# Performance work log

Measured on AMD Instinct MI355X. Metric: run time of the kernel, lower is better.

The kernel has to match this reference:

```python
import jax, jax.numpy as jnp
import numpy as np

D_MODEL = 1024
NUM_HEADS = 16
HEAD_DIM = D_MODEL // NUM_HEADS
B, T = 4, 2048


def setup_inputs() -> dict:
    key = jax.random.key(0)
    ks = jax.random.split(key, 11)
    s = 0.02
    return {
        "q": jax.random.normal(ks[0], (B, T, D_MODEL), jnp.float32),
        "k": jax.random.normal(ks[1], (B, T, D_MODEL), jnp.float32),
        "v": jax.random.normal(ks[2], (B, T, D_MODEL), jnp.float32),
        "Wq": jax.random.normal(ks[3], (D_MODEL, D_MODEL), jnp.float32) * s,
        "bq": jnp.zeros((D_MODEL,), jnp.float32),
        "Wk": jax.random.normal(ks[4], (D_MODEL, D_MODEL), jnp.float32) * s,
        "bk": jnp.zeros((D_MODEL,), jnp.float32),
        "Wv": jax.random.normal(ks[5], (D_MODEL, D_MODEL), jnp.float32) * s,
        "bv": jnp.zeros((D_MODEL,), jnp.float32),
        "Wo": jax.random.normal(ks[6], (D_MODEL, D_MODEL), jnp.float32) * s,
        "bo": jnp.zeros((D_MODEL,), jnp.float32),
    }


def reference(q, k, v, Wq, bq, Wk, bk, Wv, bv, Wo, bo):
    Bq, Tq, _ = q.shape
    Tk = k.shape[1]
    # Linear projections then split heads: [B, H, T, Dh]
    qh = (q @ Wq + bq).reshape(Bq, Tq, NUM_HEADS, HEAD_DIM).transpose(0, 2, 1, 3)
    kh = (k @ Wk + bk).reshape(Bq, Tk, NUM_HEADS, HEAD_DIM).transpose(0, 2, 1, 3)
    vh = (v @ Wv + bv).reshape(Bq, Tk, NUM_HEADS, HEAD_DIM).transpose(0, 2, 1, 3)
    scale = 1.0 / jnp.sqrt(jnp.asarray(HEAD_DIM, qh.dtype))
    scores = jnp.einsum("bhqd,bhkd->bhqk", qh, kh) * scale  # [B,H,Tq,Tk]
    attn = jax.nn.softmax(scores, axis=-1)
    # dropout p=0.0 (eval) -> identity
    out = jnp.einsum("bhqk,bhkd->bhqd", attn, vh)  # [B,H,Tq,Dh]
    out = out.transpose(0, 2, 1, 3).reshape(Bq, Tq, D_MODEL)
    return out @ Wo + bo
```

## Files before the change

kernel.cpp:

```cpp
#include <hip/hip_runtime.h>
#include <cstdint>

#define DEV static __device__ __forceinline__

typedef unsigned short u16;
typedef unsigned int u32;
typedef __attribute__((ext_vector_type(8))) _Float16 half8;
typedef __attribute__((ext_vector_type(4))) float f32x4;
typedef __attribute__((ext_vector_type(4))) unsigned short u16x4;

DEV u16 f2h_bits(float f) {
  _Float16 h = (_Float16)f;
  union { _Float16 h; u16 u; } cv; cv.h = h; return cv.u;
}

DEV u32 pack2h(float a, float b) {
  union { __fp16 __attribute__((ext_vector_type(2))) h; u32 u; } cv;
  cv.h = __builtin_amdgcn_cvt_pkrtz(a, b);
  return cv.u;
}

#define EXP2 __builtin_amdgcn_exp2f

DEV void async_cp16(const void* g, void* l) {
  __builtin_amdgcn_global_load_lds(
      (const __attribute__((address_space(1))) void*)g,
      (__attribute__((address_space(3))) void*)l, 16, 0, 0);
}

__global__ void cvt_f16(const float4* __restrict__ in, u16* __restrict__ out) {
  const int i = blockIdx.x * 256 + threadIdx.x;
  float4 f = in[i];
  u16x4 u;
  u.x = f2h_bits(f.x); u.y = f2h_bits(f.y); u.z = f2h_bits(f.z); u.w = f2h_bits(f.w);
  *(u16x4*)(out + i * 4) = u;
}

struct TParams { const float* W[4]; u16* out[4]; };

__global__ void tcvt4(TParams p) {
  __shared__ float tile[32][33];
  const int w = blockIdx.x >> 10;
  const int bidx = blockIdx.x & 1023;
  const float* __restrict__ Wf = p.W[w];
  u16* __restrict__ Wt = p.out[w];
  const int bx = bidx & 31, by = bidx >> 5;
  const int tx = threadIdx.x & 31, ty = threadIdx.x >> 5;
#pragma unroll
  for (int r = 0; r < 32; r += 8)
    tile[ty + r][tx] = Wf[(by * 32 + ty + r) * 1024 + bx * 32 + tx];
  __syncthreads();
#pragma unroll
  for (int r = 0; r < 32; r += 8)
    Wt[(bx * 32 + ty + r) * 1024 + by * 32 + tx] = f2h_bits(tile[tx][ty + r]);
}

template<int EPI, typename OutT>
DEV void gemm_body(const u16* __restrict__ A, const u16* __restrict__ Bt,
                   const float* __restrict__ bias, OutT* __restrict__ out,
                   u16 (*As)[8192], u16 (*Bs)[8192])
{
  const int tid = threadIdx.x;
  const int wave = tid >> 6, lane = tid & 63;
  const int l15 = lane & 15, lg = lane >> 4;
  const int bid = ((blockIdx.x & 7) << 6) | (blockIdx.x >> 3);
  const int bm = bid >> 3, bn = bid & 7;
  const int m0 = bm * 128, n0 = bn * 128;
  const int wr = wave >> 1, wc = wave & 1;

  const f32x4 fz = {0.f, 0.f, 0.f, 0.f};
  f32x4 acc[4][4];
#pragma unroll
  for (int m = 0; m < 4; ++m)
#pragma unroll
    for (int n = 0; n < 4; ++n) acc[m][n] = fz;

  const char* srcA[4]; const char* srcB[4]; int dstAB[4];
#pragma unroll
  for (int j = 0; j < 4; ++j) {
    const int x = (j * 256 + tid) * 16;
    const int row = x >> 7, colb = x & 127;
    const int pc = colb ^ ((row & 7) << 4);
    srcA[j] = (const char*)A  + (size_t)(m0 + row) * 2048 + pc;
    srcB[j] = (const char*)Bt + (size_t)(n0 + row) * 2048 + pc;
    dstAB[j] = x;
  }

#define STAGE_G(buf, T)                                                     \
  do {                                                                      \
    _Pragma("unroll") for (int j = 0; j < 4; ++j)                           \
      async_cp16(srcA[j] + (size_t)(T) * 128, (char*)As[buf] + dstAB[j]);   \
    _Pragma("unroll") for (int j = 0; j < 4; ++j)                           \
      async_cp16(srcB[j] + (size_t)(T) * 128, (char*)Bs[buf] + dstAB[j]);   \
  } while (0)

  STAGE_G(0, 0);
  asm volatile("s_waitcnt vmcnt(0)" ::: "memory");
  __builtin_amdgcn_s_barrier();
  __builtin_amdgcn_sched_barrier(0);

#define GEMM_IT(T, BR, BS)                                                  \
  do {                                                                      \
    if ((T) < 15) STAGE_G(BS, (T) + 1);                                     \
    half8 af[2][4], bf[2][4];                                               \
    _Pragma("unroll") for (int kk = 0; kk < 2; ++kk)                        \
      _Pragma("unroll") for (int m = 0; m < 4; ++m) {                       \
        const int row = wr * 64 + m * 16 + l15;                             \
        af[kk][m] = *(const half8*)((const char*)As[BR] +                   \
            ((row * 128 + kk * 64 + lg * 16) ^ ((row & 7) << 4)));          \
      }                                                                     \
    _Pragma("unroll") for (int kk = 0; kk < 2; ++kk)                        \
      _Pragma("unroll") for (int n = 0; n < 4; ++n) {                       \
        const int row = wc * 64 + n * 16 + l15;                             \
        bf[kk][n] = *(const half8*)((const char*)Bs[BR] +                   \
            ((row * 128 + kk * 64 + lg * 16) ^ ((row & 7) << 4)));          \
      }                                                                     \
    _Pragma("unroll") for (int kk = 0; kk < 2; ++kk)                        \
      _Pragma("unroll") for (int m = 0; m < 4; ++m)                         \
        _Pragma("unroll") for (int n = 0; n < 4; ++n)                       \
          acc[m][n] = __builtin_amdgcn_mfma_f32_16x16x32_f16(af[kk][m], bf[kk][n], acc[m][n], 0, 0, 0); \
    if ((T) < 15) {                                                         \
      asm volatile("s_waitcnt vmcnt(0)" ::: "memory");                      \
      __builtin_amdgcn_s_barrier();                                         \
      __builtin_amdgcn_sched_barrier(0);                                    \
    }                                                                       \
  } while (0)

  for (int tb = 0; tb < 16; tb += 2) {
    GEMM_IT(tb,     0, 1);
    GEMM_IT(tb + 1, 1, 0);
  }
#undef GEMM_IT
#undef STAGE_G

#pragma unroll
  for (int m = 0; m < 4; ++m) {
    const int Rb = m0 + wr * 64 + m * 16 + lg * 4;
#pragma unroll
    for (int n = 0; n < 4; ++n) {
      const int C = n0 + wc * 64 + n * 16 + l15;
      const float bv = bias[C];
#pragma unroll
      for (int i = 0; i < 4; ++i) {
        const int R = Rb + i;
        const float vv = acc[m][n][i] + bv;
        if (EPI == 3) {
          ((float*)out)[(size_t)R * 1024 + C] = vv;
        } else {
          const int b = R >> 11, t = R & 2047, hh = C >> 6, d = C & 63;
          if (EPI == 0)
            ((u16*)out)[((b * 16 + hh) * 2048 + t) * 64 + d] = f2h_bits(vv * 0.18033688f);
          else if (EPI == 1)
            ((u16*)out)[((b * 16 + hh) * 2048 + t) * 64 + d] = f2h_bits(vv);
          else
            ((u16*)out)[((b * 16 + hh) * 64 + d) * 2048 + t] = f2h_bits(vv);
        }
      }
    }
  }
}

template<int EPI>
__launch_bounds__(256, 2)
__global__ void gemm_proj(const u16* __restrict__ A, const u16* __restrict__ Bt,
                          const float* __restrict__ bias, u16* __restrict__ out)
{
  __shared__ u16 As[2][8192];
  __shared__ u16 Bs[2][8192];
  gemm_body<EPI, u16>(A, Bt, bias, out, As, Bs);
}

__launch_bounds__(256, 2)
__global__ void gemm_o(const u16* __restrict__ A, const u16* __restrict__ Bt,
                       const float* __restrict__ bias, float* __restrict__ out)
{
  __shared__ u16 As[2][8192];
  __shared__ u16 Bs[2][8192];
  gemm_body<3, float>(A, Bt, bias, out, As, Bs);
}

__launch_bounds__(512)
__global__ void attn_kernel(const u16* __restrict__ qh, const u16* __restrict__ kh,
                            const u16* __restrict__ vt, u16* __restrict__ O)
{
  __shared__ u16 SM[32768];
  const int tid = threadIdx.x, wave = tid >> 6, lane = tid & 63;
  const int l15 = lane & 15, lg = lane >> 4;
  const int swz = ((blockIdx.x & 7) << 6) | (blockIdx.x >> 3);
  const int bh = swz >> 3;
  const int q0 = (swz & 7) << 8;
  const int b = bh >> 4, h = bh & 15;

  const char* qbase = (const char*)(qh + (size_t)(bh * 2048 + q0) * 64);
  const char* kbase = (const char*)(kh + (size_t)bh * 2048 * 64);
  const char* vbase = (const char*)(vt + (size_t)bh * 64 * 2048);

  char* Kbuf[4] = { (char*)SM,         (char*)SM + 8192,
                    (char*)SM + 16384, (char*)SM + 24576 };
  char* Vbuf[4] = { (char*)SM + 32768, (char*)SM + 40960,
                    (char*)SM + 49152, (char*)SM + 57344 };

  const bool isK = wave < 4;
  const char* ksrc[2]; int kdst[2];
  const char* vsrc[2]; int vdstA[2], vdstB[2];
#pragma unroll
  for (int j = 0; j < 2; ++j) {
    if (isK) {
      const int yb = wave * 2048 + j * 1024 + lane * 16;
      const int row = yb >> 7;
      ksrc[j] = kbase + (yb ^ ((row & 7) << 4));
      kdst[j] = yb;
      vsrc[j] = nullptr; vdstA[j] = vdstB[j] = 0;
    } else {
      const int u = (wave - 4) * 128 + j * 64 + lane;
      const int d = u >> 3, a = u & 7;
      vsrc[j] = vbase + (size_t)d * 4096 + a * 16;
      const int n = a >> 1;
      const int s1 = 32 * (n >> 1) + 16 * (a & 1) + 4 * (n & 1);
      const int sw = (d & 7) << 4;
      vdstA[j] = (d * 128 + 2 * s1) ^ sw;
      vdstB[j] = (d * 128 + 2 * s1 + 16) ^ sw;
      ksrc[j] = nullptr; kdst[j] = 0;
    }
  }

#pragma unroll
  for (int j = 0; j < 4; ++j) {
    const int x = j * 8192 + tid * 16;
    const int row = x >> 7;
    async_cp16(qbase + (x ^ ((row & 7) << 4)), (char*)SM + x);
  }
  __syncthreads();
  half8 aq[2][2];
#pragma unroll
  for (int G = 0; G < 2; ++G) {
    const int qr = wave * 32 + G * 16 + l15;
#pragma unroll
    for (int hh = 0; hh < 2; ++hh) {
      const int addr = (qr * 128 + hh * 64 + lg * 16) ^ ((qr & 7) << 4);
      aq[G][hh] = *(const half8*)((const char*)SM + addr);
    }
  }
  asm volatile("s_waitcnt lgkmcnt(0)" ::: "memory");
  __syncthreads();

  uint4 va[2][2];
  if (isK) {
    async_cp16(ksrc[0], Kbuf[0] + kdst[0]);
    async_cp16(ksrc[1], Kbuf[0] + kdst[1]);
    async_cp16(ksrc[0] + 8192, Kbuf[1] + kdst[0]);
    async_cp16(ksrc[1] + 8192, Kbuf[1] + kdst[1]);
    asm volatile("s_waitcnt vmcnt(0)" ::: "memory");
  } else {
#pragma unroll
    for (int tt = 0; tt < 2; ++tt)
#pragma unroll
      for (int j = 0; j < 2; ++j) {
        uint4 v = *(const uint4*)(vsrc[j] + (size_t)tt * 128);
        uint2 w0; w0.x = v.x; w0.y = v.y;
        uint2 w1; w1.x = v.z; w1.y = v.w;
        *(uint2*)(Vbuf[tt] + vdstA[j]) = w0;
        *(uint2*)(Vbuf[tt] + vdstB[j]) = w1;
      }
#pragma unroll
    for (int j = 0; j < 2; ++j) {
      va[0][j] = *(const uint4*)(vsrc[j] + 2 * 128);
      va[1][j] = *(const uint4*)(vsrc[j] + 3 * 128);
    }
    asm volatile("s_waitcnt lgkmcnt(0)" ::: "memory");
  }
  __builtin_amdgcn_s_barrier();
  __builtin_amdgcn_sched_barrier(0);

  half8 ones;
#pragma unroll
  for (int i = 0; i < 8; ++i) ones[i] = (_Float16)1.0f;

  const f32x4 fz = {0.f, 0.f, 0.f, 0.f};
  f32x4 o[4][2], osum[2];
#pragma unroll
  for (int i = 0; i < 4; ++i) { o[i][0] = fz; o[i][1] = fz; }
  osum[0] = fz; osum[1] = fz;

#define ATTN_TILE(BT)                                                           \
  do {                                                                          \
    f32x4 s[4][2];                                                              \
    __builtin_amdgcn_s_setprio(1);                                              \
    _Pragma("unroll") for (int n = 0; n < 4; ++n) {                             \
      const int krow = n * 16 + l15;                                            \
      const int a0 = (krow * 128 + lg * 16) ^ ((krow & 7) << 4);                \
      half8 bk0 = *(const half8*)(Kbuf[BT] + a0);                               \
      half8 bk1 = *(const half8*)(Kbuf[BT] + (a0 ^ 64));                        \
      s[n][0] = __builtin_amdgcn_mfma_f32_16x16x32_f16(bk0, aq[0][0], fz, 0, 0, 0); \
      s[n][0] = __builtin_amdgcn_mfma_f32_16x16x32_f16(bk1, aq[0][1], s[n][0], 0, 0, 0); \
      s[n][1] = __builtin_amdgcn_mfma_f32_16x16x32_f16(bk0, aq[1][0], fz, 0, 0, 0); \
      s[n][1] = __builtin_amdgcn_mfma_f32_16x16x32_f16(bk1, aq[1][1], s[n][1], 0, 0, 0); \
    }                                                                           \
    __builtin_amdgcn_s_setprio(0);                                              \
    half8 pa[2][2];                                                             \
    _Pragma("unroll") for (int G = 0; G < 2; ++G)                               \
      _Pragma("unroll") for (int hh = 0; hh < 2; ++hh) {                        \
        union { u32 w[4]; half8 hv; } cv;                                       \
        cv.w[0] = pack2h(EXP2(s[2*hh][G][0]),   EXP2(s[2*hh][G][1]));           \
        cv.w[1] = pack2h(EXP2(s[2*hh][G][2]),   EXP2(s[2*hh][G][3]));           \
        cv.w[2] = pack2h(EXP2(s[2*hh+1][G][0]), EXP2(s[2*hh+1][G][1]));         \
        cv.w[3] = pack2h(EXP2(s[2*hh+1][G][2]), EXP2(s[2*hh+1][G][3]));         \
        pa[G][hh] = cv.hv;                                                      \
      }                                                                         \
    __builtin_amdgcn_s_setprio(1);                                              \
    _Pragma("unroll") for (int G = 0; G < 2; ++G) {                             \
      osum[G] = __builtin_amdgcn_mfma_f32_16x16x32_f16(pa[G][0], ones, osum[G], 0, 0, 0); \
      osum[G] = __builtin_amdgcn_mfma_f32_16x16x32_f16(pa[G][1], ones, osum[G], 0, 0, 0); \
    }                                                                           \
    _Pragma("unroll") for (int nd = 0; nd < 4; ++nd) {                          \
      const int dr = nd * 16 + l15;                                             \
      const int a0 = (dr * 128 + lg * 16) ^ ((dr & 7) << 4);                    \
      half8 bv0 = *(const half8*)(Vbuf[BT] + a0);                               \
      half8 bv1 = *(const half8*)(Vbuf[BT] + (a0 ^ 64));                        \
      o[nd][0] = __builtin_amdgcn_mfma_f32_16x16x32_f16(pa[0][0], bv0, o[nd][0], 0, 0, 0); \
      o[nd][0] = __builtin_amdgcn_mfma_f32_16x16x32_f16(pa[0][1], bv1, o[nd][0], 0, 0, 0); \
      o[nd][1] = __builtin_amdgcn_mfma_f32_16x16x32_f16(pa[1][0], bv0, o[nd][1], 0, 0, 0); \
      o[nd][1] = __builtin_amdgcn_mfma_f32_16x16x32_f16(pa[1][1], bv1, o[nd][1], 0, 0, 0); \
    }                                                                           \
    __builtin_amdgcn_s_setprio(0);                                              \
  } while (0)

#define PERIOD(P, C0, C1, S0, S1, DOSTAGE, DOVA, DOBAR)                         \
  do {                                                                          \
    if (isK) {                                                                  \
      if (DOSTAGE) {                                                            \
        async_cp16(ksrc[0] + (size_t)(2*(P)+2) * 8192, Kbuf[S0] + kdst[0]);     \
        async_cp16(ksrc[1] + (size_t)(2*(P)+2) * 8192, Kbuf[S0] + kdst[1]);     \
        async_cp16(ksrc[0] + (size_t)(2*(P)+3) * 8192, Kbuf[S1] + kdst[0]);     \
        async_cp16(ksrc[1] + (size_t)(2*(P)+3) * 8192, Kbuf[S1] + kdst[1]);     \
      }                                                                         \
    } else {                                                                    \
      if (DOSTAGE) {                                                            \
        _Pragma("unroll") for (int j = 0; j < 2; ++j) {                         \
          uint2 w0, w1;                                                         \
          w0.x = va[0][j].x; w0.y = va[0][j].y;                                 \
          w1.x = va[0][j].z; w1.y = va[0][j].w;                                 \
          *(uint2*)(Vbuf[S0] + vdstA[j]) = w0;                                  \
          *(uint2*)(Vbuf[S0] + vdstB[j]) = w1;                                  \
          w0.x = va[1][j].x; w0.y = va[1][j].y;                                 \
          w1.x = va[1][j].z; w1.y = va[1][j].w;                                 \
          *(uint2*)(Vbuf[S1] + vdstA[j]) = w0;                                  \
          *(uint2*)(Vbuf[S1] + vdstB[j]) = w1;                                  \
        }                                                                       \
        if (DOVA) {                                                             \
          _Pragma("unroll") for (int j = 0; j < 2; ++j) {                       \
            va[0][j] = *(const uint4*)(vsrc[j] + (size_t)(2*(P)+4) * 128);      \
            va[1][j] = *(const uint4*)(vsrc[j] + (size_t)(2*(P)+5) * 128);      \
          }                                                                     \
        }                                                                       \
      }                                                                         \
    }                                                                           \
    ATTN_TILE(C0);                                                              \
    ATTN_TILE(C1);                                                              \
    if (DOBAR) {                                                                \
      if (isK) asm volatile("s_waitcnt vmcnt(0)" ::: "memory");                 \
      else     asm volatile("s_waitcnt lgkmcnt(0)" ::: "memory");               \
      __builtin_amdgcn_s_barrier();                                             \
      __builtin_amdgcn_sched_barrier(0);                                        \
    }                                                                           \
  } while (0)

  for (int pb = 0; pb < 14; pb += 2) {
    PERIOD(pb,     0, 1, 2, 3, 1, 1, 1);
    PERIOD(pb + 1, 2, 3, 0, 1, 1, 1, 1);
  }
  PERIOD(14, 0, 1, 2, 3, 1, 0, 1);
  PERIOD(15, 2, 3, 0, 1, 0, 0, 0);
#undef PERIOD
#undef ATTN_TILE

#pragma unroll
  for (int G = 0; G < 2; ++G)
#pragma unroll
    for (int i = 0; i < 4; ++i) {
      const float inv = 1.f / osum[G][i];
      const int t = q0 + wave * 32 + G * 16 + lg * 4 + i;
      u16* orow = O + ((size_t)(b * 2048 + t)) * 1024 + h * 64;
#pragma unroll
      for (int nd = 0; nd < 4; ++nd)
        orow[nd * 16 + l15] = f2h_bits(o[nd][G][i] * inv);
    }
}

extern "C" void kernel_launch(void* const* d_in, const int* in_sizes, int n_in,
                              void* d_out, int out_size, void* d_ws, size_t ws_size,
                              hipStream_t stream)
{
  const float* q  = (const float*)d_in[0];
  const float* k  = (const float*)d_in[1];
  const float* v  = (const float*)d_in[2];
  const float* Wq = (const float*)d_in[3];
  const float* bq = (const float*)d_in[4];
  const float* Wk = (const float*)d_in[5];
  const float* bk = (const float*)d_in[6];
  const float* Wv = (const float*)d_in[7];
  const float* bv = (const float*)d_in[8];
  const float* Wo = (const float*)d_in[9];
  const float* bo = (const float*)d_in[10];

  u16* W = (u16*)d_ws;
  const unsigned MB = 1u << 20;
  u16* wtq = W + 0 * MB;
  u16* wtk = W + 1 * MB;
  u16* wtv = W + 2 * MB;
  u16* wto = W + 3 * MB;
  u16* qhb = W + 4 * MB;
  u16* khb = W + 12 * MB;
  u16* vtb = W + 20 * MB;
  u16* Xb  = W + 28 * MB;

  TParams tp;
  tp.W[0] = Wq; tp.W[1] = Wk; tp.W[2] = Wv; tp.W[3] = Wo;
  tp.out[0] = wtq; tp.out[1] = wtk; tp.out[2] = wtv; tp.out[3] = wto;
  tcvt4<<<4096, 256, 0, stream>>>(tp);

  cvt_f16<<<8192, 256, 0, stream>>>((const float4*)q, Xb);
  gemm_proj<0><<<512, 256, 0, stream>>>(Xb, wtq, bq, qhb);
  cvt_f16<<<8192, 256, 0, stream>>>((const float4*)k, Xb);
  gemm_proj<1><<<512, 256, 0, stream>>>(Xb, wtk, bk, khb);
  cvt_f16<<<8192, 256, 0, stream>>>((const float4*)v, Xb);
  gemm_proj<2><<<512, 256, 0, stream>>>(Xb, wtv, bv, vtb);

  attn_kernel<<<512, 512, 0, stream>>>(qhb, khb, vtb, Xb);

  gemm_o<<<512, 256, 0, stream>>>(Xb, wto, bo, (float*)d_out);
}
```

Measured before the change: 204.6 us.

## Double query rows per attention block to reuse K/V tiles across more queries

Each attention block now handles 512 query rows instead of 256, with every wave owning 64 rows (four 16-row groups) rather than 32. The grid shrinks from 512 to 256 blocks, so each K/V tile staged in shared memory feeds twice as many MFMAs and total K/V traffic is halved. Score computation is split into two half-passes to limit live registers. In exchange, register pressure rises with more accumulators, and 256 blocks may underfill a GPU with 256 CUs, reducing parallelism and latency hiding.

```diff
diff --git a/kernel.cpp b/kernel.cpp
--- a/kernel.cpp
+++ b/kernel.cpp
@@ -186,9 +186,9 @@
   __shared__ u16 SM[32768];
   const int tid = threadIdx.x, wave = tid >> 6, lane = tid & 63;
   const int l15 = lane & 15, lg = lane >> 4;
-  const int swz = ((blockIdx.x & 7) << 6) | (blockIdx.x >> 3);
-  const int bh = swz >> 3;
-  const int q0 = (swz & 7) << 8;
+  const int swz = ((blockIdx.x & 7) << 5) | (blockIdx.x >> 3);
+  const int bh = swz >> 2;
+  const int q0 = (swz & 3) << 9;
   const int b = bh >> 4, h = bh & 15;
 
   const char* qbase = (const char*)(qh + (size_t)(bh * 2048 + q0) * 64);
@@ -225,16 +225,16 @@
   }
 
 #pragma unroll
-  for (int j = 0; j < 4; ++j) {
+  for (int j = 0; j < 8; ++j) {
     const int x = j * 8192 + tid * 16;
     const int row = x >> 7;
     async_cp16(qbase + (x ^ ((row & 7) << 4)), (char*)SM + x);
   }
   __syncthreads();
-  half8 aq[2][2];
-#pragma unroll
-  for (int G = 0; G < 2; ++G) {
-    const int qr = wave * 32 + G * 16 + l15;
+  half8 aq[4][2];
+#pragma unroll
+  for (int G = 0; G < 4; ++G) {
+    const int qr = wave * 64 + G * 16 + l15;
 #pragma unroll
     for (int hh = 0; hh < 2; ++hh) {
       const int addr = (qr * 128 + hh * 64 + lg * 16) ^ ((qr & 7) << 4);
@@ -277,38 +277,52 @@
   for (int i = 0; i < 8; ++i) ones[i] = (_Float16)1.0f;
 
   const f32x4 fz = {0.f, 0.f, 0.f, 0.f};
-  f32x4 o[4][2], osum[2];
-#pragma unroll
-  for (int i = 0; i < 4; ++i) { o[i][0] = fz; o[i][1] = fz; }
-  osum[0] = fz; osum[1] = fz;
+  f32x4 o[4][4], osum[4];
+#pragma unroll
+  for (int i = 0; i < 4; ++i) {
+#pragma unroll
+    for (int G = 0; G < 4; ++G) o[i][G] = fz;
+    osum[i] = fz;
+  }
 
 #define ATTN_TILE(BT)                                                           \
   do {                                                                          \
-    f32x4 s[4][2];                                                              \
+    half8 pa[4][2];                                                             \
+    _Pragma("unroll") for (int hp = 0; hp < 2; ++hp) {                          \
+      f32x4 s0[4], s1[4];                                                       \
+      __builtin_amdgcn_s_setprio(1);                                            \
+      {                                                                         \
+        const int krow = (2 * hp) * 16 + l15;                                   \
+        const int a0 = (krow * 128 + lg * 16) ^ ((krow & 7) << 4);              \
+        half8 bk0 = *(const half8*)(Kbuf[BT] + a0);                             \
+        half8 bk1 = *(const half8*)(Kbuf[BT] + (a0 ^ 64));                      \
+        _Pragma("unroll") for (int G = 0; G < 4; ++G) {                         \
+          s0[G] = __builtin_amdgcn_mfma_f32_16x16x32_f16(bk0, aq[G][0], fz, 0, 0, 0); \
+          s0[G] = __builtin_amdgcn_mfma_f32_16x16x32_f16(bk1, aq[G][1], s0[G], 0, 0, 0); \
+        }                                                                       \
+      }                                                                         \
+      {                                                                         \
+        const int krow = (2 * hp + 1) * 16 + l15;                               \
+        const int a0 = (krow * 128 + lg * 16) ^ ((krow & 7) << 4);              \
+        half8 bk0 = *(const half8*)(Kbuf[BT] + a0);                             \
+        half8 bk1 = *(const half8*)(Kbuf[BT] + (a0 ^ 64));                      \
+        _Pragma("unroll") for (int G = 0; G < 4; ++G) {                         \
+          s1[G] = __builtin_amdgcn_mfma_f32_16x16x32_f16(bk0, aq[G][0], fz, 0, 0, 0); \
+          s1[G] = __builtin_amdgcn_mfma_f32_16x16x32_f16(bk1, aq[G][1], s1[G], 0, 0, 0); \
+        }                                                                       \
+      }                                                                         \
+      __builtin_amdgcn_s_setprio(0);                                            \
+      _Pragma("unroll") for (int G = 0; G < 4; ++G) {                           \
+        union { u32 w[4]; half8 hv; } cv;                                       \
+        cv.w[0] = pack2h(EXP2(s0[G][0]), EXP2(s0[G][1]));                       \
+        cv.w[1] = pack2h(EXP2(s0[G][2]), EXP2(s0[G][3]));                       \
+        cv.w[2] = pack2h(EXP2(s1[G][0]), EXP2(s1[G][1]));                       \
+        cv.w[3] = pack2h(EXP2(s1[G][2]), EXP2(s1[G][3]));                       \
+        pa[G][hp] = cv.hv;                                                      \
+      }                                                                         \
+    }                                                                           \
     __builtin_amdgcn_s_setprio(1);                                              \
-    _Pragma("unroll") for (int n = 0; n < 4; ++n) {                             \
-      const int krow = n * 16 + l15;                                            \
-      const int a0 = (krow * 128 + lg * 16) ^ ((krow & 7) << 4);                \
-      half8 bk0 = *(const half8*)(Kbuf[BT] + a0);                               \
-      half8 bk1 = *(const half8*)(Kbuf[BT] + (a0 ^ 64));                        \
-      s[n][0] = __builtin_amdgcn_mfma_f32_16x16x32_f16(bk0, aq[0][0], fz, 0, 0, 0); \
-      s[n][0] = __builtin_amdgcn_mfma_f32_16x16x32_f16(bk1, aq[0][1], s[n][0], 0, 0, 0); \
-      s[n][1] = __builtin_amdgcn_mfma_f32_16x16x32_f16(bk0, aq[1][0], fz, 0, 0, 0); \
-      s[n][1] = __builtin_amdgcn_mfma_f32_16x16x32_f16(bk1, aq[1][1], s[n][1], 0, 0, 0); \
-    }                                                                           \
-    __builtin_amdgcn_s_setprio(0);                                              \
-    half8 pa[2][2];                                                             \
-    _Pragma("unroll") for (int G = 0; G < 2; ++G)                               \
-      _Pragma("unroll") for (int hh = 0; hh < 2; ++hh) {                        \
-        union { u32 w[4]; half8 hv; } cv;                                       \
-        cv.w[0] = pack2h(EXP2(s[2*hh][G][0]),   EXP2(s[2*hh][G][1]));           \
-        cv.w[1] = pack2h(EXP2(s[2*hh][G][2]),   EXP2(s[2*hh][G][3]));           \
-        cv.w[2] = pack2h(EXP2(s[2*hh+1][G][0]), EXP2(s[2*hh+1][G][1]));         \
-        cv.w[3] = pack2h(EXP2(s[2*hh+1][G][2]), EXP2(s[2*hh+1][G][3]));         \
-        pa[G][hh] = cv.hv;                                                      \
-      }                                                                         \
-    __builtin_amdgcn_s_setprio(1);                                              \
-    _Pragma("unroll") for (int G = 0; G < 2; ++G) {                             \
+    _Pragma("unroll") for (int G = 0; G < 4; ++G) {                             \
       osum[G] = __builtin_amdgcn_mfma_f32_16x16x32_f16(pa[G][0], ones, osum[G], 0, 0, 0); \
       osum[G] = __builtin_amdgcn_mfma_f32_16x16x32_f16(pa[G][1], ones, osum[G], 0, 0, 0); \
     }                                                                           \
@@ -317,10 +331,10 @@
       const int a0 = (dr * 128 + lg * 16) ^ ((dr & 7) << 4);                    \
       half8 bv0 = *(const half8*)(Vbuf[BT] + a0);                               \
       half8 bv1 = *(const half8*)(Vbuf[BT] + (a0 ^ 64));                        \
-      o[nd][0] = __builtin_amdgcn_mfma_f32_16x16x32_f16(pa[0][0], bv0, o[nd][0], 0, 0, 0); \
-      o[nd][0] = __builtin_amdgcn_mfma_f32_16x16x32_f16(pa[0][1], bv1, o[nd][0], 0, 0, 0); \
-      o[nd][1] = __builtin_amdgcn_mfma_f32_16x16x32_f16(pa[1][0], bv0, o[nd][1], 0, 0, 0); \
-      o[nd][1] = __builtin_amdgcn_mfma_f32_16x16x32_f16(pa[1][1], bv1, o[nd][1], 0, 0, 0); \
+      _Pragma("unroll") for (int G = 0; G < 4; ++G) {                           \
+        o[nd][G] = __builtin_amdgcn_mfma_f32_16x16x32_f16(pa[G][0], bv0, o[nd][G], 0, 0, 0); \
+        o[nd][G] = __builtin_amdgcn_mfma_f32_16x16x32_f16(pa[G][1], bv1, o[nd][G], 0, 0, 0); \
+      }                                                                         \
     }                                                                           \
     __builtin_amdgcn_s_setprio(0);                                              \
   } while (0)
@@ -375,11 +389,11 @@
 #undef ATTN_TILE
 
 #pragma unroll
-  for (int G = 0; G < 2; ++G)
+  for (int G = 0; G < 4; ++G)
 #pragma unroll
     for (int i = 0; i < 4; ++i) {
       const float inv = 1.f / osum[G][i];
-      const int t = q0 + wave * 32 + G * 16 + lg * 4 + i;
+      const int t = q0 + wave * 64 + G * 16 + lg * 4 + i;
       u16* orow = O + ((size_t)(b * 2048 + t)) * 1024 + h * 64;
 #pragma unroll
       for (int nd = 0; nd < 4; ++nd)
@@ -426,7 +440,7 @@
   cvt_f16<<<8192, 256, 0, stream>>>((const float4*)v, Xb);
   gemm_proj<2><<<512, 256, 0, stream>>>(Xb, wtv, bv, vtb);
 
-  attn_kernel<<<512, 512, 0, stream>>>(qhb, khb, vtb, Xb);
+  attn_kernel<<<256, 512, 0, stream>>>(qhb, khb, vtb, Xb);
 
   gemm_o<<<512, 256, 0, stream>>>(Xb, wto, bo, (float*)d_out);
 }
```

After: 200.2 us. 2.2% less time.
